# Optimization experiments

Measured on AMD Instinct MI355X. Metric: run time of the kernel, lower is better.

Reference implementation:

```python
import jax, jax.numpy as jnp
import numpy as np

B, N, NQ, C = 4, 16384, 1024, 128
NS = 64          # nsample
RADIUS = 0.3     # ball-query fallback radius


def setup_inputs() -> dict:
    key = jax.random.key(0)
    k1, k2, k3, k4 = jax.random.split(key, 4)
    key_xyz = jax.random.uniform(k1, (B, N, 3), dtype=jnp.float32)
    key_features = jax.random.normal(k2, (B, C, N), dtype=jnp.float32)
    centers = jax.random.uniform(k3, (B, NQ, 3), dtype=jnp.float32)
    # box sizes L/H/W in [0.05, 0.25]
    sizes = 0.05 + 0.2 * jax.random.uniform(k4, (B, NQ, 3), dtype=jnp.float32)
    query_xyz = jnp.concatenate([centers, sizes], axis=-1)
    return {"key_xyz": key_xyz, "key_features": key_features, "query_xyz": query_xyz}


def _box_group(key_xyz, key_features, query_xyz):
    centers = query_xyz[:, :, :3]              # [B,nq,3]
    half = 0.5 * query_xyz[:, :, 3:]           # [B,nq,3] half box extents

    # per-query per-key absolute offsets: [B,nq,N,3]
    d = jnp.abs(key_xyz[:, None, :, :] - centers[:, :, None, :])
    inside = jnp.all(d <= half[:, :, None, :], axis=-1)      # [B,nq,N] AABB test
    dist2 = jnp.sum(d * d, axis=-1)                          # [B,nq,N]

    # ball-query fallback for queries whose box contains no point
    has_box = jnp.any(inside, axis=-1)                       # [B,nq]
    sel = jnp.where(has_box[..., None], inside, dist2 <= RADIUS * RADIUS)

    # first NS selected indices (stable sort puts selected points first,
    # preserving ascending key index order -> deterministic box_query semantics)
    order = jnp.argsort((~sel).astype(jnp.int32), axis=-1)[:, :, :NS]  # [B,nq,NS]

    count = jnp.minimum(jnp.sum(sel, axis=-1), NS)           # [B,nq]
    pad = jnp.arange(NS)[None, None, :] >= count[..., None]  # True = padded slot
    idx = jnp.where(pad, 0, order)                           # pad with index 0
    mask = pad.at[:, :, 0].set(False)                        # cuda path: mask[...,0]=False

    # gathers
    g_xyz = jax.vmap(lambda k, i: k[i])(key_xyz, idx)        # [B,nq,NS,3]
    g_xyz = g_xyz - centers[:, :, None, :]                   # recenter on query
    grouped_xyz = jnp.transpose(g_xyz, (0, 3, 1, 2))         # [B,3,nq,NS]
    grouped_feat = jax.vmap(lambda f, i: f[:, i])(key_features, idx)  # [B,C,nq,NS]
    return grouped_xyz, grouped_feat, mask


def reference(key_xyz, key_features, query_xyz):
    return _box_group(key_xyz, key_features, query_xyz)
```

## Files before the change

### kernel.cpp

```cpp
#include <hip/hip_runtime.h>

#pragma clang fp contract(off)

#define B_  4
#define N_  16384
#define NQ_ 1024
#define C_  128
#define NS_ 64
#define G_  16
#define NCELL_ 4096
#define MAXCELLS_ 344
#define SELCAP_ 1024

#define OFF_FEAT   ((size_t)0)
#define SZ_FEAT    ((size_t)B_*N_*C_*4)
#define OFF_COUNTS (OFF_FEAT + SZ_FEAT)
#define OFF_CSTART (OFF_COUNTS + (size_t)B_*NCELL_*4)
#define OFF_CURSOR (OFF_CSTART + (size_t)B_*NCELL_*4)
#define OFF_PLIST4 (OFF_CURSOR + (size_t)B_*NCELL_*4)
#define WS_NEED    (OFF_PLIST4 + (size_t)B_*N_*16)

__device__ __forceinline__ int cell_of(float x, float y, float z) {
    int ix = (int)(x * (float)G_); ix = min(G_ - 1, max(0, ix));
    int iy = (int)(y * (float)G_); iy = min(G_ - 1, max(0, iy));
    int iz = (int)(z * (float)G_); iz = min(G_ - 1, max(0, iz));
    return ix + (iy << 4) + (iz << 8);
}

__global__ __launch_bounds__(256) void zero_k(int* __restrict__ counts) {
    int id = blockIdx.x * 256 + threadIdx.x;
    if (id < B_ * NCELL_) counts[id] = 0;
}

__global__ __launch_bounds__(256) void bin_count_k(const float* __restrict__ key_xyz,
                                                   int* __restrict__ counts) {
    int id = blockIdx.x * 256 + threadIdx.x;
    int b = id >> 14, n = id & (N_ - 1);
    const float* p = key_xyz + ((size_t)b * N_ + n) * 3;
    int cid = cell_of(p[0], p[1], p[2]);
    atomicAdd(&counts[(b << 12) + cid], 1);
}

__global__ __launch_bounds__(1024) void scan_k(const int* __restrict__ counts,
                                               int* __restrict__ cstart,
                                               int* __restrict__ cursor) {
    __shared__ int a[1024];
    int b = blockIdx.x, t = threadIdx.x;
    int base = b << 12;
    int c0 = t * 4;
    int v0 = counts[base + c0 + 0], v1 = counts[base + c0 + 1];
    int v2 = counts[base + c0 + 2], v3 = counts[base + c0 + 3];
    int s = v0 + v1 + v2 + v3;
    a[t] = s;
    __syncthreads();
    for (int o = 1; o < 1024; o <<= 1) {
        int add = (t >= o) ? a[t - o] : 0;
        __syncthreads();
        a[t] += add;
        __syncthreads();
    }
    int excl = a[t] - s;
    int e0 = excl, e1 = e0 + v0, e2 = e1 + v1, e3 = e2 + v2;
    cstart[base + c0 + 0] = e0; cursor[base + c0 + 0] = e0;
    cstart[base + c0 + 1] = e1; cursor[base + c0 + 1] = e1;
    cstart[base + c0 + 2] = e2; cursor[base + c0 + 2] = e2;
    cstart[base + c0 + 3] = e3; cursor[base + c0 + 3] = e3;
}

#define TBLK_ (B_ * (C_/32) * (N_/32))
__global__ __launch_bounds__(256) void scatter_transpose_k(
    const float* __restrict__ key_xyz, const float* __restrict__ key_feat,
    int* __restrict__ cursor, float4* __restrict__ plist4,
    float* __restrict__ feat_t)
{
    __shared__ float ttile[32][33];
    int t = threadIdx.x;
    if (blockIdx.x < TBLK_) {
        int id2 = blockIdx.x;
        int b   = id2 >> 11;
        int rem = id2 & 2047;
        int c0  = (rem >> 9) * 32;
        int n0  = (rem & 511) * 32;
        int x = t & 31, y = t >> 5;
#pragma unroll
        for (int k = 0; k < 4; ++k)
            ttile[y + 8*k][x] = __builtin_nontemporal_load(
                &key_feat[((size_t)b * C_ + c0 + y + 8*k) * N_ + n0 + x]);
        __syncthreads();
#pragma unroll
        for (int k = 0; k < 4; ++k)
            feat_t[((size_t)b * N_ + n0 + y + 8*k) * C_ + c0 + x] = ttile[x][y + 8*k];
        return;
    }
    int id = (blockIdx.x - TBLK_) * 256 + t;
    int b = id >> 14, n = id & (N_ - 1);
    const float* p = key_xyz + ((size_t)b * N_ + n) * 3;
    float x = p[0], y = p[1], z = p[2];
    int cid = cell_of(x, y, z);
    int pos = atomicAdd(&cursor[(b << 12) + cid], 1);
    plist4[(b << 14) + pos] = make_float4(x, y, z, __int_as_float(n));
}

__global__ __launch_bounds__(512) void selgather_k(
    const float* __restrict__ key_xyz, const float* __restrict__ query,
    const int* __restrict__ counts, const int* __restrict__ cstart,
    const float4* __restrict__ plist4, const float* __restrict__ feat_t,
    float* __restrict__ out_xyz, float* __restrict__ out_feat,
    float* __restrict__ out_mask)
{
    __shared__ int   s_ccnt[MAXCELLS_];
    __shared__ int   s_cstart[MAXCELLS_];
    __shared__ int   s_pref[MAXCELLS_ + 1];
    __shared__ int   s_sel[SELCAP_];
    __shared__ int   s_scnt;
    __shared__ int   s_list[8][NS_];
    __shared__ int   s_cnt8[8];
    __shared__ int   s_idx[NS_];
    __shared__ int   s_count;
    __shared__ float tile[NS_][65];

    int i    = blockIdx.x;
    int xcd  = i & 7;
    int b    = xcd >> 1;
    int q    = ((i >> 3) << 1) | (xcd & 1);
    int bq   = (b << 10) | q;
    int t    = threadIdx.x;
    int wave = t >> 6, lane = t & 63;

    const float* qp = query + (size_t)bq * 6;
    float cx = qp[0], cy = qp[1], cz = qp[2];
    float hx = 0.5f * qp[3], hy = 0.5f * qp[4], hz = 0.5f * qp[5];
    const float* kb = key_xyz + (size_t)b * N_ * 3;

    if (t == 0) s_scnt = 0;

    int ilox = max(0, (int)floorf((cx - hx) * (float)G_) - 1);
    int ihix = min(G_ - 1, (int)floorf((cx + hx) * (float)G_) + 1);
    int iloy = max(0, (int)floorf((cy - hy) * (float)G_) - 1);
    int ihiy = min(G_ - 1, (int)floorf((cy + hy) * (float)G_) + 1);
    int iloz = max(0, (int)floorf((cz - hz) * (float)G_) - 1);
    int ihiz = min(G_ - 1, (int)floorf((cz + hz) * (float)G_) + 1);
    int nx = ihix - ilox + 1, ny = ihiy - iloy + 1, nz = ihiz - iloz + 1;
    int ncells = nx * ny * nz;

    for (int ci = t; ci < ncells; ci += 512) {
        int iz = ci / (nx * ny);
        int r  = ci - iz * (nx * ny);
        int iy = r / nx;
        int ix = r - iy * nx;
        int cid = (ilox + ix) + ((iloy + iy) << 4) + ((iloz + iz) << 8);
        s_ccnt[ci]   = counts[(b << 12) + cid];
        s_cstart[ci] = cstart[(b << 12) + cid];
    }
    __syncthreads();

    if (wave == 0) {
        int run = 0;
        for (int base = 0; base < ncells; base += 64) {
            int x = (base + lane < ncells) ? s_ccnt[base + lane] : 0;
            int own = x;
#pragma unroll
            for (int o = 1; o < 64; o <<= 1) {
                int v = __shfl_up(x, (unsigned)o);
                if (lane >= o) x += v;
            }
            if (base + lane < ncells) s_pref[base + lane] = run + x - own;
            run += __shfl(x, 63);
        }
        if (lane == 0) s_pref[ncells] = run;
    }
    __syncthreads();

    int total = s_pref[ncells];
    const float4* pl = plist4 + ((size_t)b << 14);
    for (int ii = t; ii < total; ii += 512) {
        int lo = 0, hi = ncells;
        while (hi - lo > 1) {
            int mid = (lo + hi) >> 1;
            if (s_pref[mid] <= ii) lo = mid; else hi = mid;
        }
        float4 p = pl[s_cstart[lo] + (ii - s_pref[lo])];
        float dx = fabsf(p.x - cx);
        float dy = fabsf(p.y - cy);
        float dz = fabsf(p.z - cz);
        if (dx <= hx && dy <= hy && dz <= hz) {
            int pos = atomicAdd(&s_scnt, 1);
            if (pos < SELCAP_) s_sel[pos] = __float_as_int(p.w);
        }
    }
    __syncthreads();
    int scnt = min(s_scnt, SELCAP_);

    if (scnt > 0) {
        int count = min(scnt, NS_);
        if (scnt <= NS_) {
            if (wave == 0) {
                int v = (lane < scnt) ? s_sel[lane] : 0x7fffffff;
#pragma unroll
                for (int k = 2; k <= 64; k <<= 1) {
                    for (int j = k >> 1; j > 0; j >>= 1) {
                        int pv = __shfl_xor(v, (unsigned)j);
                        bool dir   = (lane & k) == 0;
                        bool lower = (lane & j) == 0;
                        int mn = min(v, pv), mx = max(v, pv);
                        v = dir ? (lower ? mn : mx) : (lower ? mx : mn);
                    }
                }
                s_idx[lane] = (lane < count) ? v : 0;
                if (lane == 0) s_count = count;
            }
        } else {
            int m = NS_;
            while (m < scnt) m <<= 1;
            for (int ii = t; ii < m; ii += 512)
                if (ii >= scnt) s_sel[ii] = 0x7fffffff;
            __syncthreads();
            for (int k = 2; k <= m; k <<= 1) {
                for (int j = k >> 1; j > 0; j >>= 1) {
                    for (int ii = t; ii < m; ii += 512) {
                        int ixj = ii ^ j;
                        if (ixj > ii) {
                            int va = s_sel[ii], vb = s_sel[ixj];
                            bool up = ((ii & k) == 0);
                            if ((va > vb) == up) { s_sel[ii] = vb; s_sel[ixj] = va; }
                        }
                    }
                    __syncthreads();
                }
            }
            if (t < NS_) s_idx[t] = (t < count) ? s_sel[t] : 0;
            if (t == 0)  s_count = count;
        }
    } else {
        const float R2 = (float)(0.3 * 0.3);
        const int seg = N_ / 8;
        int n0s = wave * seg;
        unsigned long long ltm = (1ull << lane) - 1ull;
        int cnt = 0;
        for (int it = 0; it < seg / 64; ++it) {
            int n = n0s + it * 64 + lane;
            float dx = kb[3*n + 0] - cx;
            float dy = kb[3*n + 1] - cy;
            float dz = kb[3*n + 2] - cz;
            float d2 = dx*dx + dy*dy + dz*dz;
            bool r = d2 <= R2;
            unsigned long long mm = __ballot(r);
            if (r) {
                int p = cnt + __popcll(mm & ltm);
                if (p < NS_) s_list[wave][p] = n;
            }
            cnt += __popcll(mm);
            if (cnt >= NS_) break;
        }
        if (lane == 0) s_cnt8[wave] = cnt;
        __syncthreads();
        if (wave == 0) {
            int tot = 0;
#pragma unroll
            for (int w = 0; w < 8; ++w) tot += s_cnt8[w];
            int count = min(tot, NS_);
            int j = lane;
            int idx = 0;
            if (j < count) {
                int w = 0, rem = j;
                while (rem >= s_cnt8[w]) { rem -= s_cnt8[w]; ++w; }
                idx = s_list[w][rem];
            }
            s_idx[j] = idx;
            if (lane == 0) s_count = count;
        }
    }
    __syncthreads();

    int count = s_count;
    if (t < NS_) {
        int j = t, idx = s_idx[j];
        out_mask[(size_t)bq * NS_ + j] = (j >= count && j > 0) ? 1.0f : 0.0f;
        float px = kb[3*idx + 0] - cx;
        float py = kb[3*idx + 1] - cy;
        float pz = kb[3*idx + 2] - cz;
        size_t xb = ((size_t)b * 3) * NQ_ * NS_ + (size_t)q * NS_ + j;
        out_xyz[xb]                       = px;
        out_xyz[xb +     (size_t)NQ_*NS_] = py;
        out_xyz[xb + 2 * (size_t)NQ_*NS_] = pz;
    }

    const float4* ft4 = (const float4*)feat_t + (size_t)b * N_ * (C_ / 4);
    float* ob = out_feat + (size_t)b * C_ * NQ_ * NS_ + (size_t)q * NS_;
#pragma unroll
    for (int chunk = 0; chunk < 2; ++chunk) {
#pragma unroll
        for (int k = 0; k < 2; ++k) {
            int u  = t + k * 512;
            int j  = u >> 4;
            int c4 = u & 15;
            float4 v = ft4[(size_t)s_idx[j] * (C_ / 4) + chunk * 16 + c4];
            tile[j][c4*4 + 0] = v.x;
            tile[j][c4*4 + 1] = v.y;
            tile[j][c4*4 + 2] = v.z;
            tile[j][c4*4 + 3] = v.w;
        }
        __syncthreads();
#pragma unroll
        for (int r = 0; r < 8; ++r) {
            int cl = wave + r * 8;
            __builtin_nontemporal_store(tile[lane][cl],
                &ob[(size_t)(chunk * 64 + cl) * (NQ_ * NS_) + lane]);
        }
        __syncthreads();
    }
}

__global__ __launch_bounds__(256) void select_lin_k(
    const float* __restrict__ key_xyz, const float* __restrict__ query,
    int* __restrict__ idx_out, float* __restrict__ out_xyz,
    float* __restrict__ out_mask)
{
    int bq = blockIdx.x;
    int b  = bq >> 10;
    int q  = bq & (NQ_ - 1);
    int t    = threadIdx.x;
    int wave = t >> 6;
    int lane = t & 63;

    __shared__ int s_list[4][NS_];
    __shared__ int s_cnt[4];

    const float* qp = query + (size_t)bq * 6;
    float cx = qp[0], cy = qp[1], cz = qp[2];
    float hx = 0.5f * qp[3], hy = 0.5f * qp[4], hz = 0.5f * qp[5];
    const float* kb = key_xyz + (size_t)b * N_ * 3;

    const int seg = N_ / 4;
    int n0 = wave * seg;
    unsigned long long lt = (1ull << lane) - 1ull;

    int cnt = 0;
    for (int it = 0; it < seg / 64; ++it) {
        int n = n0 + it * 64 + lane;
        float dx = fabsf(kb[3*n + 0] - cx);
        float dy = fabsf(kb[3*n + 1] - cy);
        float dz = fabsf(kb[3*n + 2] - cz);
        bool inside = (dx <= hx) && (dy <= hy) && (dz <= hz);
        unsigned long long m = __ballot(inside);
        if (inside) {
            int p = cnt + __popcll(m & lt);
            if (p < NS_) s_list[wave][p] = n;
        }
        cnt += __popcll(m);
        if (cnt >= NS_) break;
    }
    if (lane == 0) s_cnt[wave] = cnt;
    __syncthreads();

    int ti = s_cnt[0] + s_cnt[1] + s_cnt[2] + s_cnt[3];
    if (ti == 0) {
        const float R2 = (float)(0.3 * 0.3);
        cnt = 0;
        for (int it = 0; it < seg / 64; ++it) {
            int n = n0 + it * 64 + lane;
            float dx = kb[3*n + 0] - cx;
            float dy = kb[3*n + 1] - cy;
            float dz = kb[3*n + 2] - cz;
            float d2 = dx*dx + dy*dy + dz*dz;
            bool r = d2 <= R2;
            unsigned long long m = __ballot(r);
            if (r) {
                int p = cnt + __popcll(m & lt);
                if (p < NS_) s_list[wave][p] = n;
            }
            cnt += __popcll(m);
            if (cnt >= NS_) break;
        }
        if (lane == 0) s_cnt[wave] = cnt;
    }
    __syncthreads();

    if (wave == 0) {
        int c0s = min(s_cnt[0], NS_);
        int c1s = min(s_cnt[1], NS_);
        int c2s = min(s_cnt[2], NS_);
        int tot   = s_cnt[0] + s_cnt[1] + s_cnt[2] + s_cnt[3];
        int count = min(tot, NS_);
        int j = lane;
        int idx = 0;
        if (j < count) {
            int o1 = c0s, o2 = o1 + c1s, o3 = o2 + c2s;
            if      (j < o1) idx = s_list[0][j];
            else if (j < o2) idx = s_list[1][j - o1];
            else if (j < o3) idx = s_list[2][j - o2];
            else             idx = s_list[3][j - o3];
        }
        idx_out[(size_t)bq * NS_ + j] = idx;
        out_mask[(size_t)bq * NS_ + j] = (j >= count && j > 0) ? 1.0f : 0.0f;
        float px = kb[3*idx + 0] - cx;
        float py = kb[3*idx + 1] - cy;
        float pz = kb[3*idx + 2] - cz;
        size_t xb = ((size_t)b * 3) * NQ_ * NS_ + (size_t)q * NS_ + j;
        out_xyz[xb]                       = px;
        out_xyz[xb +     (size_t)NQ_*NS_] = py;
        out_xyz[xb + 2 * (size_t)NQ_*NS_] = pz;
    }
}

__global__ __launch_bounds__(256) void gather_direct_k(
    const int* __restrict__ idx_in, const float* __restrict__ key_feat,
    float* __restrict__ out_feat)
{
    int bq = blockIdx.x;
    int b  = bq >> 10;
    int q  = bq & (NQ_ - 1);
    int t    = threadIdx.x;
    int wave = t >> 6;
    int lane = t & 63;
    __shared__ int s_idx[NS_];
    if (t < NS_) s_idx[t] = idx_in[(size_t)bq * NS_ + t];
    __syncthreads();
    const float* fb = key_feat + (size_t)b * C_ * N_;
    float* ob = out_feat + (size_t)b * C_ * NQ_ * NS_ + (size_t)q * NS_;
    int idx = s_idx[lane];
    for (int c = wave; c < C_; c += 4)
        ob[(size_t)c * NQ_ * NS_ + lane] = fb[(size_t)c * N_ + idx];
}

extern "C" void kernel_launch(void* const* d_in, const int* in_sizes, int n_in,
                              void* d_out, int out_size, void* d_ws, size_t ws_size,
                              hipStream_t stream) {
    const float* key_xyz  = (const float*)d_in[0];
    const float* key_feat = (const float*)d_in[1];
    const float* query    = (const float*)d_in[2];

    float* out      = (float*)d_out;
    float* out_xyz  = out;
    float* out_feat = out + (size_t)B_ * 3 * NQ_ * NS_;
    float* out_mask = out_feat + (size_t)B_ * C_ * NQ_ * NS_;

    char* ws = (char*)d_ws;
    float*  ft      = (float*)(ws + OFF_FEAT);
    int*    counts  = (int*)(ws + OFF_COUNTS);
    int*    cstartp = (int*)(ws + OFF_CSTART);
    int*    cursor  = (int*)(ws + OFF_CURSOR);
    float4* plist4  = (float4*)(ws + OFF_PLIST4);

    if (ws_size >= WS_NEED) {
        zero_k<<<dim3((B_ * NCELL_ + 255) / 256), dim3(256), 0, stream>>>(counts);
        bin_count_k<<<dim3(B_ * N_ / 256), dim3(256), 0, stream>>>(key_xyz, counts);
        scan_k<<<dim3(B_), dim3(1024), 0, stream>>>(counts, cstartp, cursor);
        scatter_transpose_k<<<dim3(TBLK_ + B_ * N_ / 256), dim3(256), 0, stream>>>(
            key_xyz, key_feat, cursor, plist4, ft);
        selgather_k<<<dim3(B_ * NQ_), dim3(512), 0, stream>>>(
            key_xyz, query, counts, cstartp, plist4, ft,
            out_xyz, out_feat, out_mask);
    } else {
        int* d_idx = (int*)d_ws;
        select_lin_k<<<dim3(B_ * NQ_), dim3(256), 0, stream>>>(
            key_xyz, query, d_idx, out_xyz, out_mask);
        gather_direct_k<<<dim3(B_ * NQ_), dim3(256), 0, stream>>>(
            d_idx, key_feat, out_feat);
    }
}
```

Measured before the change: 211.0 us.

## Add per-wave sort plus rank merge for mid-size selections and pack cell info

```diff
diff --git a/kernel.cpp b/kernel.cpp
--- a/kernel.cpp
+++ b/kernel.cpp
@@ -15,9 +15,9 @@
 #define OFF_FEAT   ((size_t)0)
 #define SZ_FEAT    ((size_t)B_*N_*C_*4)
 #define OFF_COUNTS (OFF_FEAT + SZ_FEAT)
-#define OFF_CSTART (OFF_COUNTS + (size_t)B_*NCELL_*4)
-#define OFF_CURSOR (OFF_CSTART + (size_t)B_*NCELL_*4)
-#define OFF_PLIST4 (OFF_CURSOR + (size_t)B_*NCELL_*4)
+#define OFF_CURSOR (OFF_COUNTS + (size_t)B_*NCELL_*4)
+#define OFF_CINFO  (OFF_CURSOR + (size_t)B_*NCELL_*4)
+#define OFF_PLIST4 (OFF_CINFO + (size_t)B_*NCELL_*8)
 #define WS_NEED    (OFF_PLIST4 + (size_t)B_*N_*16)
 
 __device__ __forceinline__ int cell_of(float x, float y, float z) {
@@ -25,11 +25,6 @@
     int iy = (int)(y * (float)G_); iy = min(G_ - 1, max(0, iy));
     int iz = (int)(z * (float)G_); iz = min(G_ - 1, max(0, iz));
     return ix + (iy << 4) + (iz << 8);
-}
-
-__global__ __launch_bounds__(256) void zero_k(int* __restrict__ counts) {
-    int id = blockIdx.x * 256 + threadIdx.x;
-    if (id < B_ * NCELL_) counts[id] = 0;
 }
 
 __global__ __launch_bounds__(256) void bin_count_k(const float* __restrict__ key_xyz,
@@ -42,29 +37,40 @@
 }
 
 __global__ __launch_bounds__(1024) void scan_k(const int* __restrict__ counts,
-                                               int* __restrict__ cstart,
+                                               int2* __restrict__ cinfo,
                                                int* __restrict__ cursor) {
-    __shared__ int a[1024];
+    __shared__ int wsum[16];
     int b = blockIdx.x, t = threadIdx.x;
+    int wave = t >> 6, lane = t & 63;
     int base = b << 12;
-    int c0 = t * 4;
+    int c0 = t << 2;
     int v0 = counts[base + c0 + 0], v1 = counts[base + c0 + 1];
     int v2 = counts[base + c0 + 2], v3 = counts[base + c0 + 3];
     int s = v0 + v1 + v2 + v3;
-    a[t] = s;
-    __syncthreads();
-    for (int o = 1; o < 1024; o <<= 1) {
-        int add = (t >= o) ? a[t - o] : 0;
-        __syncthreads();
-        a[t] += add;
-        __syncthreads();
-    }
-    int excl = a[t] - s;
-    int e0 = excl, e1 = e0 + v0, e2 = e1 + v1, e3 = e2 + v2;
-    cstart[base + c0 + 0] = e0; cursor[base + c0 + 0] = e0;
-    cstart[base + c0 + 1] = e1; cursor[base + c0 + 1] = e1;
-    cstart[base + c0 + 2] = e2; cursor[base + c0 + 2] = e2;
-    cstart[base + c0 + 3] = e3; cursor[base + c0 + 3] = e3;
+    int x = s;
+#pragma unroll
+    for (int o = 1; o < 64; o <<= 1) {
+        int v = __shfl_up(x, (unsigned)o);
+        if (lane >= o) x += v;
+    }
+    if (lane == 63) wsum[wave] = x;
+    __syncthreads();
+    if (t < 16) {
+        int y = wsum[t];
+#pragma unroll
+        for (int o = 1; o < 16; o <<= 1) {
+            int v = __shfl_up(y, (unsigned)o);
+            if (t >= o) y += v;
+        }
+        wsum[t] = y;
+    }
+    __syncthreads();
+    int off = (wave ? wsum[wave - 1] : 0) + x - s;
+    int e0 = off, e1 = e0 + v0, e2 = e1 + v1, e3 = e2 + v2;
+    cinfo[base + c0 + 0] = make_int2(v0, e0); cursor[base + c0 + 0] = e0;
+    cinfo[base + c0 + 1] = make_int2(v1, e1); cursor[base + c0 + 1] = e1;
+    cinfo[base + c0 + 2] = make_int2(v2, e2); cursor[base + c0 + 2] = e2;
+    cinfo[base + c0 + 3] = make_int2(v3, e3); cursor[base + c0 + 3] = e3;
 }
 
 #define TBLK_ (B_ * (C_/32) * (N_/32))
@@ -103,8 +109,8 @@
 
 __global__ __launch_bounds__(512) void selgather_k(
     const float* __restrict__ key_xyz, const float* __restrict__ query,
-    const int* __restrict__ counts, const int* __restrict__ cstart,
-    const float4* __restrict__ plist4, const float* __restrict__ feat_t,
+    const int2* __restrict__ cinfo, const float4* __restrict__ plist4,
+    const float* __restrict__ feat_t,
     float* __restrict__ out_xyz, float* __restrict__ out_feat,
     float* __restrict__ out_mask)
 {
@@ -143,14 +149,16 @@
     int nx = ihix - ilox + 1, ny = ihiy - iloy + 1, nz = ihiz - iloz + 1;
     int ncells = nx * ny * nz;
 
-    for (int ci = t; ci < ncells; ci += 512) {
-        int iz = ci / (nx * ny);
-        int r  = ci - iz * (nx * ny);
+    const int2* ci = cinfo + (b << 12);
+    for (int cc = t; cc < ncells; cc += 512) {
+        int iz = cc / (nx * ny);
+        int r  = cc - iz * (nx * ny);
         int iy = r / nx;
         int ix = r - iy * nx;
         int cid = (ilox + ix) + ((iloy + iy) << 4) + ((iloz + iz) << 8);
-        s_ccnt[ci]   = counts[(b << 12) + cid];
-        s_cstart[ci] = cstart[(b << 12) + cid];
+        int2 v = ci[cid];
+        s_ccnt[cc]   = v.x;
+        s_cstart[cc] = v.y;
     }
     __syncthreads();
 
@@ -209,6 +217,39 @@
                 s_idx[lane] = (lane < count) ? v : 0;
                 if (lane == 0) s_count = count;
             }
+        } else if (scnt <= 512) {
+            int nw = (scnt + 63) >> 6;
+            int base = wave << 6;
+            int v = (base + lane < scnt) ? s_sel[base + lane] : 0x7fffffff;
+#pragma unroll
+            for (int k = 2; k <= 64; k <<= 1) {
+                for (int j = k >> 1; j > 0; j >>= 1) {
+                    int pv = __shfl_xor(v, (unsigned)j);
+                    bool dir   = (lane & k) == 0;
+                    bool lower = (lane & j) == 0;
+                    int mn = min(v, pv), mx = max(v, pv);
+                    v = dir ? (lower ? mn : mx) : (lower ? mx : mn);
+                }
+            }
+            s_sel[base + lane] = v;
+            __syncthreads();
+            int e = s_sel[t];
+            if (t < (nw << 6) && e != 0x7fffffff) {
+                int r = lane;
+#pragma unroll
+                for (int w = 0; w < 8; ++w) {
+                    if (w == wave || w >= nw) continue;
+                    int bw = w << 6;
+                    int pos = 0;
+#pragma unroll
+                    for (int s2 = 32; s2 >= 1; s2 >>= 1)
+                        if (s_sel[bw + pos + s2 - 1] < e) pos += s2;
+                    if (s_sel[bw + pos] < e) ++pos;
+                    r += pos;
+                }
+                if (r < NS_) s_idx[r] = e;
+            }
+            if (t == 0) s_count = NS_;
         } else {
             int m = NS_;
             while (m < scnt) m <<= 1;
@@ -438,19 +479,18 @@
     char* ws = (char*)d_ws;
     float*  ft      = (float*)(ws + OFF_FEAT);
     int*    counts  = (int*)(ws + OFF_COUNTS);
-    int*    cstartp = (int*)(ws + OFF_CSTART);
     int*    cursor  = (int*)(ws + OFF_CURSOR);
+    int2*   cinfo   = (int2*)(ws + OFF_CINFO);
     float4* plist4  = (float4*)(ws + OFF_PLIST4);
 
     if (ws_size >= WS_NEED) {
-        zero_k<<<dim3((B_ * NCELL_ + 255) / 256), dim3(256), 0, stream>>>(counts);
+        hipMemsetAsync(counts, 0, (size_t)B_ * NCELL_ * 4, stream);
         bin_count_k<<<dim3(B_ * N_ / 256), dim3(256), 0, stream>>>(key_xyz, counts);
-        scan_k<<<dim3(B_), dim3(1024), 0, stream>>>(counts, cstartp, cursor);
+        scan_k<<<dim3(B_), dim3(1024), 0, stream>>>(counts, cinfo, cursor);
         scatter_transpose_k<<<dim3(TBLK_ + B_ * N_ / 256), dim3(256), 0, stream>>>(
             key_xyz, key_feat, cursor, plist4, ft);
         selgather_k<<<dim3(B_ * NQ_), dim3(512), 0, stream>>>(
-            key_xyz, query, counts, cstartp, plist4, ft,
-            out_xyz, out_feat, out_mask);
+            key_xyz, query, cinfo, plist4, ft, out_xyz, out_feat, out_mask);
     } else {
         int* d_idx = (int*)d_ws;
         select_lin_k<<<dim3(B_ * NQ_), dim3(256), 0, stream>>>(
```

Measured after the change: 203.6 us. -3.5%, faster.
